# Optimization experiments

Hardware: AMD Instinct MI355X
Metric: run time of the kernel (lower is better)

## Reference

```python
import jax, jax.numpy as jnp
import numpy as np

B, T, H, W = 8, 10, 128, 128
WIDTH, NL = 64, 4
MT, MH, MW = 4, 8, 8
H_PRED = 5
MIN_STD = 1e-4


def setup_inputs() -> dict:
    key = jax.random.key(0)
    ks = jax.random.split(key, 12)
    scale = 1.0 / (WIDTH * WIDTH)
    return {
        "frames": jax.random.uniform(ks[0], (B, T, H, W), dtype=jnp.float32),
        "times": jax.random.uniform(ks[1], (B, T), dtype=jnp.float32),
        # lift: Conv3d(c_in=2 -> width, k=1)
        "lift_w": jax.random.normal(ks[2], (WIDTH, 2), dtype=jnp.float32) * 0.5,
        "lift_b": jnp.zeros((WIDTH,), jnp.float32),
        # spectral weights: (layer, quadrant, in, out, mt, mh, mw, re/im)
        "spec_w": jax.random.uniform(ks[3], (NL, 4, WIDTH, WIDTH, MT, MH, MW, 2), dtype=jnp.float32) * scale,
        # skip 1x1 Conv3d per layer
        "skip_w": jax.random.normal(ks[4], (NL, WIDTH, WIDTH), dtype=jnp.float32) * (1.0 / np.sqrt(WIDTH)),
        "skip_b": jnp.zeros((NL, WIDTH), jnp.float32),
        # temporal aggregation Conv3d kernel (h_ctx,1,1): (out, in, T)
        "agg_w": jax.random.normal(ks[5], (WIDTH, WIDTH, T), dtype=jnp.float32) * (1.0 / np.sqrt(WIDTH * T)),
        "agg_b": jnp.zeros((WIDTH,), jnp.float32),
        "fc1_w": jax.random.normal(ks[6], (WIDTH + 2, 128), dtype=jnp.float32) * (1.0 / np.sqrt(WIDTH + 2)),
        "fc1_b": jnp.zeros((128,), jnp.float32),
        "fc2_w": jax.random.normal(ks[7], (128, 2 * H_PRED), dtype=jnp.float32) * (1.0 / np.sqrt(128)),
        "fc2_b": jnp.zeros((2 * H_PRED,), jnp.float32),
    }


def _spectral_conv(x, wl):
    # x: (B, C, T, H, W); wl: (4, C, C, MT, MH, MW, 2) real/imag
    w = wl[..., 0] + 1j * wl[..., 1]  # (4, C, C, MT, MH, MW) complex
    x_ft = jnp.fft.rfftn(x, axes=(-3, -2, -1), norm="ortho")  # (B,C,T,H,W//2+1)
    Bc, C, Tt, Hh, Wf = x_ft.shape

    def mul(blk, wq):
        return jnp.einsum("bixyz,ioxyz->boxyz", blk, wq)

    out_ft = jnp.zeros((Bc, C, Tt, Hh, Wf), dtype=x_ft.dtype)
    out_ft = out_ft.at[:, :, :MT, :MH, :MW].set(mul(x_ft[:, :, :MT, :MH, :MW], w[0]))
    out_ft = out_ft.at[:, :, :MT, Hh - MH:, :MW].set(mul(x_ft[:, :, :MT, Hh - MH:, :MW], w[1]))
    out_ft = out_ft.at[:, :, Tt - MT:, :MH, :MW].set(mul(x_ft[:, :, Tt - MT:, :MH, :MW], w[2]))
    out_ft = out_ft.at[:, :, Tt - MT:, Hh - MH:, :MW].set(mul(x_ft[:, :, Tt - MT:, Hh - MH:, :MW], w[3]))
    return jnp.fft.irfftn(out_ft, s=(Tt, x.shape[-2], x.shape[-1]), axes=(-3, -2, -1), norm="ortho")


def reference(frames, times, lift_w, lift_b, spec_w, skip_w, skip_b,
              agg_w, agg_b, fc1_w, fc1_b, fc2_w, fc2_b):
    gelu = lambda v: jax.nn.gelu(v, approximate=False)
    # feature volume: (B, 2, T, H, W) = [frames, broadcast times]
    t_feat = jnp.broadcast_to(times[:, None, :, None, None], (B, 1, T, H, W))
    feat = jnp.concatenate([frames[:, None], t_feat], axis=1)
    # lift (1x1x1 conv)
    x = jnp.einsum("bcthw,oc->bothw", feat, lift_w) + lift_b[None, :, None, None, None]
    for l in range(NL):
        sx = _spectral_conv(x, spec_w[l])
        sk = jnp.einsum("bithw,oi->bothw", x, skip_w[l]) + skip_b[l][None, :, None, None, None]
        x = gelu(sx + sk)
    # temporal aggregation: valid conv over full T -> (B, C, H, W)
    x = jnp.einsum("bithw,oit->bohw", x, agg_w) + agg_b[None, :, None, None]
    # (x, y) grid channels
    gx = jnp.broadcast_to(jnp.linspace(-1.0, 1.0, W)[None, :], (H, W))
    gy = jnp.broadcast_to(jnp.linspace(-1.0, 1.0, H)[:, None], (H, W))
    grid = jnp.broadcast_to(jnp.stack([gx, gy], 0)[None], (B, 2, H, W))
    x = jnp.concatenate([x, grid], axis=1)  # (B, C+2, H, W)
    x = jnp.transpose(x, (0, 2, 3, 1))      # (B, H, W, C+2)
    x = gelu(x @ fc1_w + fc1_b)
    out = x @ fc2_w + fc2_b                 # (B, H, W, 2*h_pred)
    mu = out[..., 0::2]
    sigma = jax.nn.softplus(out[..., 1::2]) + MIN_STD
    return jnp.concatenate([mu, sigma], axis=-1)  # (B, H, W, 2*h_pred)
```

## Files before the change

### kernel.cpp

```cpp
#include <hip/hip_runtime.h>
#include <math.h>


#define TWO_PI 6.2831853071795864769f
#define ORTHO_SC 2.4705294220065465e-3f

typedef unsigned short u16;
typedef _Float16 f16;
typedef __attribute__((ext_vector_type(8))) _Float16 f16x8;
typedef __attribute__((ext_vector_type(4))) float f32x4;

#define MFMAH(acc, a, b) acc = __builtin_amdgcn_mfma_f32_16x16x32_f16(a, b, acc, 0, 0, 0)

__device__ __forceinline__ u16 f16b(float v) {
  f16 h = (f16)v;
  return __builtin_bit_cast(u16, h);
}
__device__ __forceinline__ float f16lo(float v) {
  f16 h = (f16)v;
  return v - (float)h;
}
__device__ __forceinline__ float f16f(u16 b) {
  return (float)__builtin_bit_cast(f16, b);
}
__device__ __forceinline__ float gelu_fast(float x) {
  float u = 0.7978845608f * (x + 0.044715f * x * x * x);
  float a = fminf(u * 2.885390082f, 30.0f);
  float e = __builtin_exp2f(a);
  return x * e * __builtin_amdgcn_rcpf(e + 1.0f);
}

__global__ __launch_bounds__(256) void k_prep2(const float* __restrict__ skip_w,
                                               const float* __restrict__ agg_w,
                                               u16* __restrict__ swf,
                                               u16* __restrict__ awf,
                                               u16* __restrict__ Tt,
                                               float2* __restrict__ twf,
                                               u16* __restrict__ Ef) {
  int e = blockIdx.x*256 + threadIdx.x;
  if (e < 32768) {
    int j = e & 7, lane = (e >> 3) & 63, half = (e >> 9) & 1, ks = (e >> 10) & 1;
    int strip = (e >> 11) & 3, layer = e >> 13;
    int co = strip*16 + (lane & 15);
    int ci = ks*32 + (lane >> 4)*8 + j;
    float v = skip_w[((size_t)(layer*64) + co)*64 + ci];
    swf[e] = half ? f16b(f16lo(v)) : f16b(v);
  } else if (e < 114688) {
    int ee = e - 32768;
    int j = ee & 7, lane = (ee >> 3) & 63;
    int v9 = ee >> 9;
    int half = v9 & 1; v9 >>= 1;
    int ks = v9 & 1; v9 >>= 1;
    int t = v9 % 10, strip = v9 / 10;
    int co = strip*16 + (lane & 15);
    int ci = ks*32 + (lane >> 4)*8 + j;
    float v = agg_w[((size_t)co*64 + ci)*10 + t];
    awf[ee] = half ? f16b(f16lo(v)) : f16b(v);
  } else if (e < 122880) {
    int ee = e - 114688;
    int half = ee >> 12, r = ee & 4095, w = r >> 5, kk = r & 31;
    int m = kk >> 1;
    float val;
    if (kk >= 16) val = 0.f;
    else if (kk == 0) val = 1.f;
    else if (kk == 1) val = 0.f;
    else {
      float th = TWO_PI * (float)m * (float)w / 128.0f;
      val = (kk & 1) ? (-2.f*sinf(th)) : (2.f*cosf(th));
    }
    Tt[ee] = half ? f16b(f16lo(val)) : f16b(val);
  } else if (e < 123904) {
    int ee = e - 122880;
    int w = ee >> 3, k = ee & 7;
    float th = TWO_PI * (float)k * (float)w / 128.0f;
    twf[ee] = make_float2(cosf(th), -sinf(th));
  } else if (e < 125952) {
    int ee = e - 123904;
    int j = ee & 7, lane = (ee >> 3) & 63, kc = ee >> 9;
    int n = lane & 15, g = lane >> 4;
    int w = kc*32 + g*8 + j;
    int k = n >> 1;
    float th = TWO_PI * (float)k * (float)w / 128.0f;
    float val = (n & 1) ? (-sinf(th)) : cosf(th);
    Ef[ee] = f16b(val);
    Ef[2048 + ee] = f16b(f16lo(val));
  }
}

__global__ __launch_bounds__(128) void k_lift_fwdW(const float* __restrict__ frames,
                                                   const float* __restrict__ times,
                                                   const float* __restrict__ lift_w,
                                                   const float* __restrict__ lift_b,
                                                   const float2* __restrict__ twf,
                                                   u16* __restrict__ xT,
                                                   float* __restrict__ xw) {
  __shared__ u16 xs[64][130];
  __shared__ float2 tws[128][8];
  __shared__ float fr[128];
  __shared__ float lw0[64], lw1a[64];
  int bth = blockIdx.x;
  int h = bth & 127; int bt = bth >> 7; int t = bt % 10, b = bt / 10;
  int tid = threadIdx.x;
  for (int i = tid; i < 1024; i += 128) tws[i >> 3][i & 7] = twf[i];
  float tv = times[b*10 + t];
  fr[tid] = frames[((size_t)(b*10 + t)*128 + h)*128 + tid];
  if (tid < 64) { lw0[tid] = lift_w[2*tid]; lw1a[tid] = lift_w[2*tid+1]*tv + lift_b[tid]; }
  __syncthreads();
  {
    int w = tid;
    float f = fr[w];
    unsigned pk[32];
    #pragma unroll
    for (int q = 0; q < 32; ++q) {
      float v0 = f*lw0[2*q] + lw1a[2*q];
      float v1 = f*lw0[2*q+1] + lw1a[2*q+1];
      u16 h0 = f16b(v0), h1 = f16b(v1);
      xs[2*q][w] = h0; xs[2*q+1][w] = h1;
      pk[q] = (unsigned)h0 | ((unsigned)h1 << 16);
    }
    uint4* d4 = (uint4*)(xT + (size_t)bth*8192 + w*64);
    #pragma unroll
    for (int q = 0; q < 8; ++q)
      d4[q] = make_uint4(pk[4*q], pk[4*q+1], pk[4*q+2], pk[4*q+3]);
  }
  __syncthreads();
  {
    int lane = tid & 63, wv = tid >> 6;
    float ar[4] = {0,0,0,0}, ai[4] = {0,0,0,0};
    for (int w2 = 0; w2 < 128; ++w2) {
      float xu = f16f(xs[lane][w2]);
      #pragma unroll
      for (int kk = 0; kk < 4; ++kk) {
        float2 ew = tws[w2][wv*4 + kk];
        ar[kk] += xu*ew.x; ai[kk] += xu*ew.y;
      }
    }
    size_t row = ((size_t)(b*64 + lane)*10 + t)*128 + h;
    float4* dst = (float4*)(xw + row*16 + wv*8);
    dst[0] = make_float4(ar[0], ai[0], ar[1], ai[1]);
    dst[1] = make_float4(ar[2], ai[2], ar[3], ai[3]);
  }
}

__global__ __launch_bounds__(256) void k_fwdHT(const float2* __restrict__ xw,
                                               float2* __restrict__ xf) {
  __shared__ float2 tile[2][1024];
  __shared__ float2 tw128[128];
  int bc = blockIdx.x;
  int b = bc >> 6, c = bc & 63;
  int tid = threadIdx.x;
  if (tid < 128) {
    float s, co; sincosf(TWO_PI * (float)tid / 128.0f, &s, &co);
    tw128[tid] = make_float2(co, -s);
  }
  int tpar = tid >> 7, j = tid & 127;
  int khi = j >> 3, kwi = j & 7;
  int kh = (khi < 8) ? khi : (112 + khi);
  float accr[8], acci[8];
  #pragma unroll
  for (int k = 0; k < 8; ++k) { accr[k] = 0.f; acci[k] = 0.f; }
  for (int tt = 0; tt < 5; ++tt) {
    __syncthreads();
    for (int u = tid; u < 2048; u += 256) {
      int tg = u >> 10, idx = u & 1023;
      tile[tg][idx] = xw[((size_t)bc*10 + tg*5 + tt)*1024 + idx];
    }
    __syncthreads();
    float xr = 0.f, xi = 0.f;
    for (int h = 0; h < 128; ++h) {
      float2 v = tile[tpar][h*8 + kwi];
      float2 tw = tw128[(h*kh) & 127];
      xr += v.x*tw.x - v.y*tw.y;
      xi += v.x*tw.y + v.y*tw.x;
    }
    int t = tpar*5 + tt;
    float sb, cb; sincosf(TWO_PI * (float)t / 10.0f, &sb, &cb);
    float p_r[10], p_i[10];
    p_r[0] = 1.f; p_i[0] = 0.f; p_r[1] = cb; p_i[1] = -sb;
    #pragma unroll
    for (int k = 2; k < 10; ++k) {
      p_r[k] = p_r[k-1]*p_r[1] - p_i[k-1]*p_i[1];
      p_i[k] = p_r[k-1]*p_i[1] + p_i[k-1]*p_r[1];
    }
    #pragma unroll
    for (int kti = 0; kti < 8; ++kti) {
      int kt = (kti < 4) ? kti : kti + 2;
      accr[kti] += xr*p_r[kt] - xi*p_i[kt];
      acci[kti] += xr*p_i[kt] + xi*p_r[kt];
    }
  }
  __syncthreads();
  float2* parts = &tile[0][0];
  #pragma unroll
  for (int kti = 0; kti < 8; ++kti)
    parts[tpar*1024 + j*8 + kti] = make_float2(accr[kti], acci[kti]);
  __syncthreads();
  if (tpar == 0) {
    #pragma unroll
    for (int kti = 0; kti < 8; ++kti) {
      float2 a = parts[j*8 + kti], bq = parts[1024 + j*8 + kti];
      xf[((size_t)b*1024 + kti*128 + j)*64 + c] =
          make_float2((a.x + bq.x)*ORTHO_SC, (a.y + bq.y)*ORTHO_SC);
    }
  }
}

__global__ __launch_bounds__(256) void k_prep_w4(const float* __restrict__ spec_w,
                                                 float2* __restrict__ wT4) {
  __shared__ float2 tile[64][65];
  int blk = blockIdx.x;
  int l = blk >> 10;
  int inner = blk & 1023;
  int mc = inner & 3, ci = (inner >> 2) & 63, q = inner >> 8;
  const float2* in = (const float2*)spec_w + (size_t)l*4194304
                     + (((size_t)q*64 + ci)*64)*256 + mc*64;
  for (int i = threadIdx.x; i < 4096; i += 256) {
    int co = i >> 6, mm = i & 63;
    tile[co][mm] = in[(size_t)co*256 + mm];
  }
  __syncthreads();
  float2* out = wT4 + (size_t)l*4194304 + ((size_t)q*256 + mc*64)*4096 + (size_t)ci*64;
  for (int i = threadIdx.x; i < 4096; i += 256) {
    int mm = i >> 6, co = i & 63;
    out[(size_t)mm*4096 + co] = tile[co][mm];
  }
}

__global__ __launch_bounds__(256) void k_mix(const float2* __restrict__ xf,
                                             const float2* __restrict__ wTl,
                                             float2* __restrict__ yf) {
  __shared__ float2 xfs[8][4][64];
  int m0 = blockIdx.x * 4;
  for (int i = threadIdx.x; i < 2048; i += 256) {
    int bb = i >> 8, mi = (i >> 6) & 3, ci = i & 63;
    xfs[bb][mi][ci] = xf[((size_t)bb*1024 + m0 + mi)*64 + ci];
  }
  __syncthreads();
  int co = threadIdx.x & 63, mi = threadIdx.x >> 6;
  int m = m0 + mi;
  int kti = m >> 7, khi = (m >> 3) & 15, kwi = m & 7;
  int q = ((kti >= 4) ? 2 : 0) + ((khi >= 8) ? 1 : 0);
  int modeidx = ((kti & 3)*8 + (khi & 7))*8 + kwi;
  const float2* wp = wTl + ((size_t)q*256 + modeidx)*4096 + co;
  float accr[8], acci[8];
  #pragma unroll
  for (int bb = 0; bb < 8; ++bb) { accr[bb] = 0.f; acci[bb] = 0.f; }
  for (int ci = 0; ci < 64; ++ci) {
    float2 wv = wp[(size_t)ci*64];
    #pragma unroll
    for (int bb = 0; bb < 8; ++bb) {
      float2 xv = xfs[bb][mi][ci];
      accr[bb] += xv.x*wv.x - xv.y*wv.y;
      acci[bb] += xv.x*wv.y + xv.y*wv.x;
    }
  }
  #pragma unroll
  for (int bb = 0; bb < 8; ++bb)
    yf[((size_t)bb*64 + co)*1024 + m] = make_float2(accr[bb], acci[bb]);
}

__global__ __launch_bounds__(256) void k_invTH(const float2* __restrict__ yf,
                                               unsigned* __restrict__ zh16) {
  __shared__ float2 ybuf[1024];
  __shared__ float2 ztb[2][128];
  __shared__ float2 tw128[128];
  int bc = blockIdx.x;
  int b = bc >> 6, c = bc & 63;
  int tid = threadIdx.x;
  for (int u = tid; u < 1024; u += 256) ybuf[u] = yf[(size_t)bc*1024 + u];
  if (tid < 128) {
    float s, co; sincosf(TWO_PI * (float)tid / 128.0f, &s, &co);
    tw128[tid] = make_float2(co, s);
  }
  int tpar = tid >> 7, j = tid & 127;
  __syncthreads();
  for (int tt = 0; tt < 5; ++tt) {
    int t = tt*2 + tpar;
    {
      float sb, cb; sincosf(TWO_PI * (float)t / 10.0f, &sb, &cb);
      float p_r[10], p_i[10];
      p_r[0] = 1.f; p_i[0] = 0.f; p_r[1] = cb; p_i[1] = sb;
      #pragma unroll
      for (int k = 2; k < 10; ++k) {
        p_r[k] = p_r[k-1]*p_r[1] - p_i[k-1]*p_i[1];
        p_i[k] = p_r[k-1]*p_i[1] + p_i[k-1]*p_r[1];
      }
      float zr = 0.f, zi = 0.f;
      #pragma unroll
      for (int kti = 0; kti < 8; ++kti) {
        int kt = (kti < 4) ? kti : kti + 2;
        float2 v = ybuf[kti*128 + j];
        zr += v.x*p_r[kt] - v.y*p_i[kt];
        zi += v.x*p_i[kt] + v.y*p_r[kt];
      }
      ztb[tpar][j] = make_float2(zr*ORTHO_SC, zi*ORTHO_SC);
    }
    __syncthreads();
    {
      int h = j;
      float ar[8], ai[8];
      #pragma unroll
      for (int kw = 0; kw < 8; ++kw) { ar[kw] = 0.f; ai[kw] = 0.f; }
      #pragma unroll
      for (int khi = 0; khi < 16; ++khi) {
        int kh = (khi < 8) ? khi : (112 + khi);
        float2 tw = tw128[(h*kh) & 127];
        #pragma unroll
        for (int kw = 0; kw < 8; ++kw) {
          float2 v = ztb[tpar][khi*8 + kw];
          ar[kw] += v.x*tw.x - v.y*tw.y;
          ai[kw] += v.x*tw.y + v.y*tw.x;
        }
      }
      unsigned* dst = zh16 + (((size_t)(b*10 + t)*128 + h)*64 + c)*8;
      #pragma unroll
      for (int kw = 0; kw < 8; ++kw)
        dst[kw] = (unsigned)f16b(ar[kw]) | ((unsigned)f16b(ai[kw]) << 16);
    }
    __syncthreads();
  }
}

__global__ __launch_bounds__(256, 4) void k_invW_mfma(const u16* __restrict__ xTin,
                                                      const unsigned* __restrict__ zh16,
                                                      const u16* __restrict__ swf_l,
                                                      const u16* __restrict__ Tt,
                                                      const u16* __restrict__ Ef,
                                                      const float* __restrict__ skb,
                                                      u16* __restrict__ xTo,
                                                      float* __restrict__ xw,
                                                      int do_dft) {
  __shared__ __align__(16) char smem[20480];
  u16* B = (u16*)smem;
  u16* zAh = (u16*)(smem + 18432);
  int tid = threadIdx.x;
  int bth = blockIdx.x;
  int lane = tid & 63;
  int wq = tid >> 6;
  int cL = lane & 15;
  int g = lane >> 4;

  f16x8 Th[2], Tl[2];
  #pragma unroll
  for (int t2 = 0; t2 < 2; ++t2) {
    int wrow = wq*32 + t2*16 + cL;
    Th[t2] = *(const f16x8*)(Tt + wrow*32 + g*8);
    Tl[t2] = *(const f16x8*)(Tt + 4096 + wrow*32 + g*8);
  }
  {
    const uint4* xsrc = (const uint4*)(xTin + (size_t)bth*8192);
    for (int u = tid; u < 1024; u += 256) {
      int w = u >> 3, c = u & 7;
      ((uint4*)(B + w*72))[c] = xsrc[u];
    }
  }
  {
    const unsigned* zsrc = zh16 + (size_t)bth*512;
    for (int u = tid; u < 512; u += 256) {
      int co = u >> 3, m = u & 7;
      *(unsigned*)(zAh + co*16 + 2*m) = zsrc[u];
    }
  }
  __syncthreads();

  f32x4 acc[4][2];
  #pragma unroll
  for (int s = 0; s < 4; ++s)
    #pragma unroll
    for (int t2 = 0; t2 < 2; ++t2) acc[s][t2] = (f32x4){0.f,0.f,0.f,0.f};

  #pragma unroll
  for (int kb = 0; kb < 2; ++kb) {
    f16x8 Ah[4], Al[4];
    #pragma unroll
    for (int s = 0; s < 4; ++s) {
      Ah[s] = *(const f16x8*)(swf_l + (size_t)(s*2048 + kb*1024 + lane*8));
      Al[s] = *(const f16x8*)(swf_l + (size_t)(s*2048 + kb*1024 + 512 + lane*8));
    }
    #pragma unroll
    for (int t2 = 0; t2 < 2; ++t2) {
      int wrow = wq*32 + t2*16 + cL;
      f16x8 bh = *(const f16x8*)(B + wrow*72 + kb*32 + g*8);
      #pragma unroll
      for (int s = 0; s < 4; ++s) {
        MFMAH(acc[s][t2], Ah[s], bh);
        MFMAH(acc[s][t2], Al[s], bh);
      }
    }
  }
  {
    f16x8 Azh[4];
    f16x8 zero8 = {0,0,0,0,0,0,0,0};
    #pragma unroll
    for (int s = 0; s < 4; ++s)
      Azh[s] = (g < 2) ? *(const f16x8*)(zAh + (s*16 + cL)*16 + g*8) : zero8;
    #pragma unroll
    for (int t2 = 0; t2 < 2; ++t2) {
      #pragma unroll
      for (int s = 0; s < 4; ++s) {
        MFMAH(acc[s][t2], Azh[s], Th[t2]);
        MFMAH(acc[s][t2], Azh[s], Tl[t2]);
      }
    }
  }

  __syncthreads();
  unsigned* out32 = (unsigned*)smem;
  #pragma unroll
  for (int s = 0; s < 4; ++s) {
    float4 b4 = *(const float4*)(skb + s*16 + g*4);
    float bb[4] = {b4.x, b4.y, b4.z, b4.w};
    #pragma unroll
    for (int t2 = 0; t2 < 2; ++t2) {
      int w = wq*32 + t2*16 + cL;
      u16 gb[4];
      #pragma unroll
      for (int r = 0; r < 4; ++r) {
        float val = acc[s][t2][r] + bb[r];
        gb[r] = f16b(gelu_fast(val));
      }
      out32[(s*8 + g*2 + 0)*130 + w] = (unsigned)gb[0] | ((unsigned)gb[1] << 16);
      out32[(s*8 + g*2 + 1)*130 + w] = (unsigned)gb[2] | ((unsigned)gb[3] << 16);
    }
  }
  __syncthreads();
  {
    uint4* xdst = (uint4*)(xTo + (size_t)bth*8192);
    for (int u = tid; u < 1024; u += 256) {
      int w = u >> 3, c = u & 7;
      unsigned r0 = out32[(c*4 + 0)*130 + w];
      unsigned r1 = out32[(c*4 + 1)*130 + w];
      unsigned r2 = out32[(c*4 + 2)*130 + w];
      unsigned r3 = out32[(c*4 + 3)*130 + w];
      xdst[u] = make_uint4(r0, r1, r2, r3);
    }
  }
  if (do_dft) {
    f32x4 acc2 = (f32x4){0.f,0.f,0.f,0.f};
    int row = wq*8 + (cL >> 1);
    int sh = (cL & 1) * 16;
    #pragma unroll
    for (int kc = 0; kc < 4; ++kc) {
      const unsigned* p = out32 + row*130 + kc*32 + g*8;
      uint2 d0 = *(const uint2*)(p);
      uint2 d1 = *(const uint2*)(p + 2);
      uint2 d2 = *(const uint2*)(p + 4);
      uint2 d3 = *(const uint2*)(p + 6);
      f16x8 a;
      a[0] = __builtin_bit_cast(f16, (u16)(d0.x >> sh));
      a[1] = __builtin_bit_cast(f16, (u16)(d0.y >> sh));
      a[2] = __builtin_bit_cast(f16, (u16)(d1.x >> sh));
      a[3] = __builtin_bit_cast(f16, (u16)(d1.y >> sh));
      a[4] = __builtin_bit_cast(f16, (u16)(d2.x >> sh));
      a[5] = __builtin_bit_cast(f16, (u16)(d2.y >> sh));
      a[6] = __builtin_bit_cast(f16, (u16)(d3.x >> sh));
      a[7] = __builtin_bit_cast(f16, (u16)(d3.y >> sh));
      f16x8 eh = *(const f16x8*)(Ef + (kc*64 + lane)*8);
      f16x8 el = *(const f16x8*)(Ef + 2048 + (kc*64 + lane)*8);
      MFMAH(acc2, a, eh);
      MFMAH(acc2, a, el);
    }
    int h = bth & 127; int bt = bth >> 7; int t = bt % 10, b = bt / 10;
    #pragma unroll
    for (int r = 0; r < 4; ++r) {
      int co = wq*16 + g*4 + r;
      size_t row2 = ((size_t)(b*64 + co)*10 + t)*128 + h;
      xw[row2*16 + cL] = acc2[r];
    }
  }
}

__global__ __launch_bounds__(256) void k_agg_mfma(const u16* __restrict__ xT,
                                                  const u16* __restrict__ awf,
                                                  const float* __restrict__ agg_b,
                                                  float* __restrict__ xa) {
  __shared__ __align__(16) u16 B[128*72];
  int tid = threadIdx.x;
  int bid = blockIdx.x;
  int h = bid & 127, b = bid >> 7;
  int lane = tid & 63;
  int wq = tid >> 6;
  int cL = lane & 15;
  int g = lane >> 4;

  f32x4 acc[4][2];
  #pragma unroll
  for (int s = 0; s < 4; ++s)
    #pragma unroll
    for (int t2 = 0; t2 < 2; ++t2) acc[s][t2] = (f32x4){0.f,0.f,0.f,0.f};

  for (int t = 0; t < 10; ++t) {
    __syncthreads();
    {
      const uint4* xsrc = (const uint4*)(xT + ((size_t)(b*10 + t)*128 + h)*8192);
      for (int u = tid; u < 1024; u += 256) {
        int w = u >> 3, c = u & 7;
        ((uint4*)(B + w*72))[c] = xsrc[u];
      }
    }
    __syncthreads();
    #pragma unroll
    for (int kc = 0; kc < 2; ++kc) {
      f16x8 Ah[4], Al[4];
      #pragma unroll
      for (int s = 0; s < 4; ++s) {
        const u16* af = awf + (size_t)((s*10 + t)*4 + kc*2)*512;
        Ah[s] = *(const f16x8*)(af + lane*8);
        Al[s] = *(const f16x8*)(af + 512 + lane*8);
      }
      #pragma unroll
      for (int t2 = 0; t2 < 2; ++t2) {
        int wrow = wq*32 + t2*16 + cL;
        f16x8 bh = *(const f16x8*)(B + wrow*72 + kc*32 + g*8);
        #pragma unroll
        for (int s = 0; s < 4; ++s) {
          MFMAH(acc[s][t2], Ah[s], bh);
          MFMAH(acc[s][t2], Al[s], bh);
        }
      }
    }
  }

  #pragma unroll
  for (int s = 0; s < 4; ++s) {
    float4 b4 = *(const float4*)(agg_b + s*16 + g*4);
    float bb[4] = {b4.x, b4.y, b4.z, b4.w};
    #pragma unroll
    for (int t2 = 0; t2 < 2; ++t2) {
      int w = wq*32 + t2*16 + cL;
      #pragma unroll
      for (int r = 0; r < 4; ++r) {
        int co = s*16 + g*4 + r;
        xa[((size_t)(b*64 + co)*128 + h)*128 + w] = acc[s][t2][r] + bb[r];
      }
    }
  }
}

__global__ __launch_bounds__(128) void k_head(const float* __restrict__ xa,
                                              const float* __restrict__ fc1_w,
                                              const float* __restrict__ fc1_b,
                                              const float* __restrict__ fc2_w,
                                              const float* __restrict__ fc2_b,
                                              float* __restrict__ out) {
  __shared__ float w1[66*128];
  __shared__ float w2[128*10];
  __shared__ float b1s[128];
  __shared__ float b2s[16];
  int bid = blockIdx.x;
  int h = bid & 127, b = bid >> 7;
  int tid = threadIdx.x;
  for (int i = tid; i < 66*128; i += 128) w1[i] = fc1_w[i];
  for (int i = tid; i < 1280; i += 128) w2[i] = fc2_w[i];
  b1s[tid] = fc1_b[tid];
  if (tid < 10) b2s[tid] = fc2_b[tid];
  float v[64];
  #pragma unroll
  for (int c = 0; c < 64; ++c)
    v[c] = xa[((size_t)(b*64 + c)*128 + h)*128 + tid];
  __syncthreads();
  float gx = -1.f + 2.f*(float)tid/127.f;
  float gy = -1.f + 2.f*(float)h/127.f;
  float o2[10];
  #pragma unroll
  for (int j = 0; j < 10; ++j) o2[j] = b2s[j];
  for (int o = 0; o < 128; ++o) {
    float a = b1s[o];
    #pragma unroll
    for (int i = 0; i < 64; ++i) a += v[i]*w1[i*128 + o];
    a += gx*w1[64*128 + o] + gy*w1[65*128 + o];
    float g = gelu_fast(a);
    #pragma unroll
    for (int j = 0; j < 10; ++j) o2[j] += g*w2[o*10 + j];
  }
  float* dst = out + ((size_t)bid*128 + tid)*10;
  #pragma unroll
  for (int k = 0; k < 5; ++k) dst[k] = o2[2*k];
  #pragma unroll
  for (int k = 0; k < 5; ++k) {
    float sv = o2[2*k+1];
    float sp = fmaxf(sv, 0.f) + log1pf(expf(-fabsf(sv)));
    dst[5 + k] = sp + 1e-4f;
  }
}

extern "C" void kernel_launch(void* const* d_in, const int* in_sizes, int n_in,
                              void* d_out, int out_size, void* d_ws, size_t ws_size,
                              hipStream_t stream) {
  const float* frames = (const float*)d_in[0];
  const float* times  = (const float*)d_in[1];
  const float* lift_w = (const float*)d_in[2];
  const float* lift_b = (const float*)d_in[3];
  const float* spec_w = (const float*)d_in[4];
  const float* skip_w = (const float*)d_in[5];
  const float* skip_b = (const float*)d_in[6];
  const float* agg_w  = (const float*)d_in[7];
  const float* agg_b  = (const float*)d_in[8];
  const float* fc1_w  = (const float*)d_in[9];
  const float* fc1_b  = (const float*)d_in[10];
  const float* fc2_w  = (const float*)d_in[11];
  const float* fc2_b  = (const float*)d_in[12];
  float* out = (float*)d_out;
  char* ws = (char*)d_ws;

  size_t off = 0;
  u16*      xT  = (u16*)(ws + off);      off += (size_t)10240*8192*2;
  float*    xw  = (float*)(ws + off);    off += (size_t)655360*16*4;
  float2*   xf  = (float2*)(ws + off);   off += (size_t)8*1024*64*8;
  float2*   yf  = (float2*)(ws + off);   off += (size_t)8*1024*64*8;
  unsigned* zh16= (unsigned*)(ws + off); off += (size_t)10240*512*4;
  float*    xa  = (float*)(ws + off);    off += (size_t)8*64*128*128*4;
  float2*   wT4 = (float2*)(ws + off);   off += (size_t)4*4194304*8;
  u16*      swf = (u16*)(ws + off);      off += (size_t)32768*2;
  u16*      awf = (u16*)(ws + off);      off += (size_t)81920*2;
  u16*      Tt  = (u16*)(ws + off);      off += (size_t)8192*2;
  float2*   twf = (float2*)(ws + off);   off += (size_t)1024*8;
  u16*      Ef  = (u16*)(ws + off);      off += (size_t)4096*2;

  k_prep2<<<492, 256, 0, stream>>>(skip_w, agg_w, swf, awf, Tt, twf, Ef);
  k_prep_w4<<<4096, 256, 0, stream>>>(spec_w, wT4);
  k_lift_fwdW<<<10240, 128, 0, stream>>>(frames, times, lift_w, lift_b, twf, xT, xw);

  for (int l = 0; l < 4; ++l) {
    k_fwdHT<<<512, 256, 0, stream>>>((const float2*)xw, xf);
    k_mix<<<256, 256, 0, stream>>>(xf, wT4 + (size_t)l*4194304, yf);
    k_invTH<<<512, 256, 0, stream>>>(yf, zh16);
    k_invW_mfma<<<10240, 256, 0, stream>>>(xT, zh16, swf + (size_t)l*8192, Tt, Ef,
                                           skip_b + l*64, xT, xw, (l < 3) ? 1 : 0);
  }
  k_agg_mfma<<<1024, 256, 0, stream>>>(xT, awf, agg_b, xa);
  k_head<<<1024, 128, 0, stream>>>(xa, fc1_w, fc1_b, fc2_w, fc2_b, out);
}
```

Baseline: 1.095 ms.

## Store W-DFT intermediate in fp16, drop weight transpose, fuse aggregation with head

The W-axis DFT intermediate is now stored as packed fp16 complex instead of fp32, which halves its write and read traffic between the lift/inverse kernels and the forward H/T DFT. The separate spectral-weight transpose kernel is removed, and k_mix reads spec_w directly with a strided access per input channel. The temporal aggregation and the MLP head are fused into one kernel that keeps the aggregated features in shared memory and splits the fc1 outputs across two thread halves. Costs are lower precision in the spectral path, uncoalesced weight loads in k_mix, and fc1 weights read from global or cache instead of LDS.

```diff
diff --git a/kernel.cpp b/kernel.cpp
--- a/kernel.cpp
+++ b/kernel.cpp
@@ -93,7 +93,7 @@
                                                    const float* __restrict__ lift_b,
                                                    const float2* __restrict__ twf,
                                                    u16* __restrict__ xT,
-                                                   float* __restrict__ xw) {
+                                                   u16* __restrict__ xw16) {
   __shared__ u16 xs[64][130];
   __shared__ float2 tws[128][8];
   __shared__ float fr[128];
@@ -136,15 +136,18 @@
       }
     }
     size_t row = ((size_t)(b*64 + lane)*10 + t)*128 + h;
-    float4* dst = (float4*)(xw + row*16 + wv*8);
-    dst[0] = make_float4(ar[0], ai[0], ar[1], ai[1]);
-    dst[1] = make_float4(ar[2], ai[2], ar[3], ai[3]);
-  }
-}
-
-__global__ __launch_bounds__(256) void k_fwdHT(const float2* __restrict__ xw,
+    unsigned p0 = (unsigned)f16b(ar[0]) | ((unsigned)f16b(ai[0]) << 16);
+    unsigned p1 = (unsigned)f16b(ar[1]) | ((unsigned)f16b(ai[1]) << 16);
+    unsigned p2 = (unsigned)f16b(ar[2]) | ((unsigned)f16b(ai[2]) << 16);
+    unsigned p3 = (unsigned)f16b(ar[3]) | ((unsigned)f16b(ai[3]) << 16);
+    *(uint4*)(xw16 + row*16 + wv*8) = make_uint4(p0, p1, p2, p3);
+  }
+}
+
+__global__ __launch_bounds__(256) void k_fwdHT(const unsigned* __restrict__ xw32,
                                                float2* __restrict__ xf) {
-  __shared__ float2 tile[2][1024];
+  __shared__ unsigned tile[2][1024];
+  __shared__ float2 parts1[1024];
   __shared__ float2 tw128[128];
   int bc = blockIdx.x;
   int b = bc >> 6, c = bc & 63;
@@ -163,15 +166,17 @@
     __syncthreads();
     for (int u = tid; u < 2048; u += 256) {
       int tg = u >> 10, idx = u & 1023;
-      tile[tg][idx] = xw[((size_t)bc*10 + tg*5 + tt)*1024 + idx];
+      tile[tg][idx] = xw32[((size_t)bc*10 + tg*5 + tt)*1024 + idx];
     }
     __syncthreads();
     float xr = 0.f, xi = 0.f;
     for (int h = 0; h < 128; ++h) {
-      float2 v = tile[tpar][h*8 + kwi];
+      unsigned uv = tile[tpar][h*8 + kwi];
+      float vx = f16f((u16)uv);
+      float vy = f16f((u16)(uv >> 16));
       float2 tw = tw128[(h*kh) & 127];
-      xr += v.x*tw.x - v.y*tw.y;
-      xi += v.x*tw.y + v.y*tw.x;
+      xr += vx*tw.x - vy*tw.y;
+      xi += vx*tw.y + vy*tw.x;
     }
     int t = tpar*5 + tt;
     float sb, cb; sincosf(TWO_PI * (float)t / 10.0f, &sb, &cb);
@@ -190,44 +195,24 @@
     }
   }
   __syncthreads();
-  float2* parts = &tile[0][0];
-  #pragma unroll
-  for (int kti = 0; kti < 8; ++kti)
-    parts[tpar*1024 + j*8 + kti] = make_float2(accr[kti], acci[kti]);
+  if (tpar == 1) {
+    #pragma unroll
+    for (int kti = 0; kti < 8; ++kti)
+      parts1[j*8 + kti] = make_float2(accr[kti], acci[kti]);
+  }
   __syncthreads();
   if (tpar == 0) {
     #pragma unroll
     for (int kti = 0; kti < 8; ++kti) {
-      float2 a = parts[j*8 + kti], bq = parts[1024 + j*8 + kti];
+      float2 bq = parts1[j*8 + kti];
       xf[((size_t)b*1024 + kti*128 + j)*64 + c] =
-          make_float2((a.x + bq.x)*ORTHO_SC, (a.y + bq.y)*ORTHO_SC);
-    }
-  }
-}
-
-__global__ __launch_bounds__(256) void k_prep_w4(const float* __restrict__ spec_w,
-                                                 float2* __restrict__ wT4) {
-  __shared__ float2 tile[64][65];
-  int blk = blockIdx.x;
-  int l = blk >> 10;
-  int inner = blk & 1023;
-  int mc = inner & 3, ci = (inner >> 2) & 63, q = inner >> 8;
-  const float2* in = (const float2*)spec_w + (size_t)l*4194304
-                     + (((size_t)q*64 + ci)*64)*256 + mc*64;
-  for (int i = threadIdx.x; i < 4096; i += 256) {
-    int co = i >> 6, mm = i & 63;
-    tile[co][mm] = in[(size_t)co*256 + mm];
-  }
-  __syncthreads();
-  float2* out = wT4 + (size_t)l*4194304 + ((size_t)q*256 + mc*64)*4096 + (size_t)ci*64;
-  for (int i = threadIdx.x; i < 4096; i += 256) {
-    int mm = i >> 6, co = i & 63;
-    out[(size_t)mm*4096 + co] = tile[co][mm];
+          make_float2((accr[kti] + bq.x)*ORTHO_SC, (acci[kti] + bq.y)*ORTHO_SC);
+    }
   }
 }
 
 __global__ __launch_bounds__(256) void k_mix(const float2* __restrict__ xf,
-                                             const float2* __restrict__ wTl,
+                                             const float* __restrict__ spec_w_l,
                                              float2* __restrict__ yf) {
   __shared__ float2 xfs[8][4][64];
   int m0 = blockIdx.x * 4;
@@ -241,12 +226,13 @@
   int kti = m >> 7, khi = (m >> 3) & 15, kwi = m & 7;
   int q = ((kti >= 4) ? 2 : 0) + ((khi >= 8) ? 1 : 0);
   int modeidx = ((kti & 3)*8 + (khi & 7))*8 + kwi;
-  const float2* wp = wTl + ((size_t)q*256 + modeidx)*4096 + co;
+  const float2* wp = (const float2*)spec_w_l
+                     + ((size_t)(q*64)*64 + co)*256 + modeidx;
   float accr[8], acci[8];
   #pragma unroll
   for (int bb = 0; bb < 8; ++bb) { accr[bb] = 0.f; acci[bb] = 0.f; }
   for (int ci = 0; ci < 64; ++ci) {
-    float2 wv = wp[(size_t)ci*64];
+    float2 wv = wp[(size_t)ci*16384];
     #pragma unroll
     for (int bb = 0; bb < 8; ++bb) {
       float2 xv = xfs[bb][mi][ci];
@@ -328,7 +314,7 @@
                                                       const u16* __restrict__ Ef,
                                                       const float* __restrict__ skb,
                                                       u16* __restrict__ xTo,
-                                                      float* __restrict__ xw,
+                                                      u16* __restrict__ xw16,
                                                       int do_dft) {
   __shared__ __align__(16) char smem[20480];
   u16* B = (u16*)smem;
@@ -465,16 +451,24 @@
     for (int r = 0; r < 4; ++r) {
       int co = wq*16 + g*4 + r;
       size_t row2 = ((size_t)(b*64 + co)*10 + t)*128 + h;
-      xw[row2*16 + cL] = acc2[r];
-    }
-  }
-}
-
-__global__ __launch_bounds__(256) void k_agg_mfma(const u16* __restrict__ xT,
+      xw16[row2*16 + cL] = f16b(acc2[r]);
+    }
+  }
+}
+
+__global__ __launch_bounds__(256) void k_agg_head(const u16* __restrict__ xT,
                                                   const u16* __restrict__ awf,
                                                   const float* __restrict__ agg_b,
-                                                  float* __restrict__ xa) {
-  __shared__ __align__(16) u16 B[128*72];
+                                                  const float* __restrict__ fc1_w,
+                                                  const float* __restrict__ fc1_b,
+                                                  const float* __restrict__ fc2_w,
+                                                  const float* __restrict__ fc2_b,
+                                                  float* __restrict__ out) {
+  __shared__ __align__(16) char smem[43520];
+  u16* B = (u16*)smem;
+  float* outx = (float*)smem;
+  float* part = (float*)(smem + 33280);
+  float* w2s  = (float*)(smem + 38400);
   int tid = threadIdx.x;
   int bid = blockIdx.x;
   int h = bid & 127, b = bid >> 7;
@@ -482,6 +476,7 @@
   int wq = tid >> 6;
   int cL = lane & 15;
   int g = lane >> 4;
+  for (int i = tid; i < 1280; i += 256) w2s[i] = fc2_w[i];
 
   f32x4 acc[4][2];
   #pragma unroll
@@ -521,6 +516,7 @@
     }
   }
 
+  __syncthreads();
   #pragma unroll
   for (int s = 0; s < 4; ++s) {
     float4 b4 = *(const float4*)(agg_b + s*16 + g*4);
@@ -531,56 +527,51 @@
       #pragma unroll
       for (int r = 0; r < 4; ++r) {
         int co = s*16 + g*4 + r;
-        xa[((size_t)(b*64 + co)*128 + h)*128 + w] = acc[s][t2][r] + bb[r];
-      }
-    }
-  }
-}
-
-__global__ __launch_bounds__(128) void k_head(const float* __restrict__ xa,
-                                              const float* __restrict__ fc1_w,
-                                              const float* __restrict__ fc1_b,
-                                              const float* __restrict__ fc2_w,
-                                              const float* __restrict__ fc2_b,
-                                              float* __restrict__ out) {
-  __shared__ float w1[66*128];
-  __shared__ float w2[128*10];
-  __shared__ float b1s[128];
-  __shared__ float b2s[16];
-  int bid = blockIdx.x;
-  int h = bid & 127, b = bid >> 7;
-  int tid = threadIdx.x;
-  for (int i = tid; i < 66*128; i += 128) w1[i] = fc1_w[i];
-  for (int i = tid; i < 1280; i += 128) w2[i] = fc2_w[i];
-  b1s[tid] = fc1_b[tid];
-  if (tid < 10) b2s[tid] = fc2_b[tid];
-  float v[64];
-  #pragma unroll
-  for (int c = 0; c < 64; ++c)
-    v[c] = xa[((size_t)(b*64 + c)*128 + h)*128 + tid];
-  __syncthreads();
-  float gx = -1.f + 2.f*(float)tid/127.f;
-  float gy = -1.f + 2.f*(float)h/127.f;
-  float o2[10];
-  #pragma unroll
-  for (int j = 0; j < 10; ++j) o2[j] = b2s[j];
-  for (int o = 0; o < 128; ++o) {
-    float a = b1s[o];
-    #pragma unroll
-    for (int i = 0; i < 64; ++i) a += v[i]*w1[i*128 + o];
-    a += gx*w1[64*128 + o] + gy*w1[65*128 + o];
-    float g = gelu_fast(a);
-    #pragma unroll
-    for (int j = 0; j < 10; ++j) o2[j] += g*w2[o*10 + j];
-  }
-  float* dst = out + ((size_t)bid*128 + tid)*10;
-  #pragma unroll
-  for (int k = 0; k < 5; ++k) dst[k] = o2[2*k];
-  #pragma unroll
-  for (int k = 0; k < 5; ++k) {
-    float sv = o2[2*k+1];
-    float sp = fmaxf(sv, 0.f) + log1pf(expf(-fabsf(sv)));
-    dst[5 + k] = sp + 1e-4f;
+        outx[co*130 + w] = acc[s][t2][r] + bb[r];
+      }
+    }
+  }
+  __syncthreads();
+
+  {
+    int w = tid & 127, oh = tid >> 7;
+    float v[64];
+    #pragma unroll
+    for (int c = 0; c < 64; ++c) v[c] = outx[c*130 + w];
+    float gx = -1.f + 2.f*(float)w/127.f;
+    float gy = -1.f + 2.f*(float)h/127.f;
+    float o2[10];
+    #pragma unroll
+    for (int j = 0; j < 10; ++j) o2[j] = 0.f;
+    int o0 = oh*64;
+    for (int o = o0; o < o0 + 64; ++o) {
+      float a = fc1_b[o];
+      #pragma unroll
+      for (int i = 0; i < 64; ++i) a += v[i]*fc1_w[i*128 + o];
+      a += gx*fc1_w[64*128 + o] + gy*fc1_w[65*128 + o];
+      float gl = gelu_fast(a);
+      #pragma unroll
+      for (int j = 0; j < 10; ++j) o2[j] += gl*w2s[o*10 + j];
+    }
+    if (oh) {
+      #pragma unroll
+      for (int j = 0; j < 10; ++j) part[w*10 + j] = o2[j];
+    }
+    __syncthreads();
+    if (!oh) {
+      float tot[10];
+      #pragma unroll
+      for (int j = 0; j < 10; ++j) tot[j] = o2[j] + part[w*10 + j] + fc2_b[j];
+      float* dst = out + ((size_t)bid*128 + w)*10;
+      #pragma unroll
+      for (int k = 0; k < 5; ++k) dst[k] = tot[2*k];
+      #pragma unroll
+      for (int k = 0; k < 5; ++k) {
+        float sv = tot[2*k+1];
+        float sp = fmaxf(sv, 0.f) + log1pf(expf(-fabsf(sv)));
+        dst[5 + k] = sp + 1e-4f;
+      }
+    }
   }
 }
 
@@ -605,12 +596,10 @@
 
   size_t off = 0;
   u16*      xT  = (u16*)(ws + off);      off += (size_t)10240*8192*2;
-  float*    xw  = (float*)(ws + off);    off += (size_t)655360*16*4;
+  u16*      xw16= (u16*)(ws + off);      off += (size_t)655360*16*2;
   float2*   xf  = (float2*)(ws + off);   off += (size_t)8*1024*64*8;
   float2*   yf  = (float2*)(ws + off);   off += (size_t)8*1024*64*8;
   unsigned* zh16= (unsigned*)(ws + off); off += (size_t)10240*512*4;
-  float*    xa  = (float*)(ws + off);    off += (size_t)8*64*128*128*4;
-  float2*   wT4 = (float2*)(ws + off);   off += (size_t)4*4194304*8;
   u16*      swf = (u16*)(ws + off);      off += (size_t)32768*2;
   u16*      awf = (u16*)(ws + off);      off += (size_t)81920*2;
   u16*      Tt  = (u16*)(ws + off);      off += (size_t)8192*2;
@@ -618,16 +607,14 @@
   u16*      Ef  = (u16*)(ws + off);      off += (size_t)4096*2;
 
   k_prep2<<<492, 256, 0, stream>>>(skip_w, agg_w, swf, awf, Tt, twf, Ef);
-  k_prep_w4<<<4096, 256, 0, stream>>>(spec_w, wT4);
-  k_lift_fwdW<<<10240, 128, 0, stream>>>(frames, times, lift_w, lift_b, twf, xT, xw);
+  k_lift_fwdW<<<10240, 128, 0, stream>>>(frames, times, lift_w, lift_b, twf, xT, xw16);
 
   for (int l = 0; l < 4; ++l) {
-    k_fwdHT<<<512, 256, 0, stream>>>((const float2*)xw, xf);
-    k_mix<<<256, 256, 0, stream>>>(xf, wT4 + (size_t)l*4194304, yf);
+    k_fwdHT<<<512, 256, 0, stream>>>((const unsigned*)xw16, xf);
+    k_mix<<<256, 256, 0, stream>>>(xf, spec_w + (size_t)l*4*64*64*256*2, yf);
     k_invTH<<<512, 256, 0, stream>>>(yf, zh16);
     k_invW_mfma<<<10240, 256, 0, stream>>>(xT, zh16, swf + (size_t)l*8192, Tt, Ef,
-                                           skip_b + l*64, xT, xw, (l < 3) ? 1 : 0);
-  }
-  k_agg_mfma<<<1024, 256, 0, stream>>>(xT, awf, agg_b, xa);
-  k_head<<<1024, 128, 0, stream>>>(xa, fc1_w, fc1_b, fc2_w, fc2_b, out);
-}
+                                           skip_b + l*64, xT, xw16, (l < 3) ? 1 : 0);
+  }
+  k_agg_head<<<1024, 256, 0, stream>>>(xT, awf, agg_b, fc1_w, fc1_b, fc2_w, fc2_b, out);
+}
```

Result: faster. 1.059 ms (-3.2%).
